# Kernel tuning notes

Measured on AMD Instinct MI355X. Metric: run time of the kernel, lower is better.

Reference implementation:

```python
import jax, jax.numpy as jnp
import numpy as np

HEADS = 16
LN_EPS = 1e-6

def _layernorm(x, scale, bias):
    mu = jnp.mean(x, axis=-1, keepdims=True)
    var = jnp.mean(jnp.square(x - mu), axis=-1, keepdims=True)
    return (x - mu) * jax.lax.rsqrt(var + LN_EPS) * scale + bias

def setup_inputs() -> dict:
    key = jax.random.key(0)
    ks = jax.random.split(key, 5)
    B, L, D, F = 2, 2048, 1024, 4096
    s = lambda fan_in: 1.0 / np.sqrt(fan_in)
    return {
        'x': jax.random.normal(ks[0], (B, L, D), jnp.float32),
        'ln1_scale': jnp.ones((D,), jnp.float32),
        'ln1_bias': jnp.zeros((D,), jnp.float32),
        'w_qkv': jax.random.normal(ks[1], (D, 3 * D), jnp.float32) * s(D),
        'w_proj': jax.random.normal(ks[2], (D, D), jnp.float32) * s(D),
        'b_proj': jnp.zeros((D,), jnp.float32),
        'ln2_scale': jnp.ones((D,), jnp.float32),
        'ln2_bias': jnp.zeros((D,), jnp.float32),
        'w_mlp1': jax.random.normal(ks[3], (D, F), jnp.float32) * s(D),
        'b_mlp1': jnp.zeros((F,), jnp.float32),
        'w_mlp2': jax.random.normal(ks[4], (F, D), jnp.float32) * s(F),
        'b_mlp2': jnp.zeros((D,), jnp.float32),
    }

def reference(x, ln1_scale, ln1_bias, w_qkv, w_proj, b_proj,
              ln2_scale, ln2_bias, w_mlp1, b_mlp1, w_mlp2, b_mlp2):
    B, L, D = x.shape
    H = HEADS
    hd = D // H
    # pre-norm attention
    h = _layernorm(x, ln1_scale, ln1_bias)
    qkv = h @ w_qkv  # [B,L,3D]
    q, k, v = jnp.split(qkv, 3, axis=-1)
    q = q.reshape(B, L, H, hd).transpose(0, 2, 1, 3)  # [B,H,L,hd]
    k = k.reshape(B, L, H, hd).transpose(0, 2, 1, 3)
    v = v.reshape(B, L, H, hd).transpose(0, 2, 1, 3)
    scale = jnp.sqrt(jnp.float32(hd))
    scores = jnp.einsum('bhqd,bhkd->bhqk', q, k) / scale  # [B,H,L,L]
    attn = jax.nn.softmax(scores, axis=-1)
    out = jnp.einsum('bhqk,bhkd->bhqd', attn, v)  # [B,H,L,hd]
    out = out.transpose(0, 2, 1, 3).reshape(B, L, D)
    x = x + out @ w_proj + b_proj
    # pre-norm MLP
    h = _layernorm(x, ln2_scale, ln2_bias)
    m = jax.nn.gelu(h @ w_mlp1 + b_mlp1, approximate=True)
    return x + m @ w_mlp2 + b_mlp2
```

## Files before the change

kernel.cpp:

```cpp
#include <hip/hip_runtime.h>
#include <hip/hip_bf16.h>
#include <cstdint>
#include <cstddef>

typedef __bf16 bf16;
typedef __bf16 bf16x8 __attribute__((ext_vector_type(8)));
typedef float f32x4 __attribute__((ext_vector_type(4)));
typedef short short4v __attribute__((ext_vector_type(4)));
typedef unsigned uint2v __attribute__((ext_vector_type(2)));

#define GLB_AS(p) ((const __attribute__((address_space(1))) unsigned*)(unsigned long long)(p))
#define LDS_AS(p) ((__attribute__((address_space(3))) unsigned*)(unsigned)(unsigned long long)(p))

__device__ __forceinline__ void g2l16(const void* g, void* l) {
  __builtin_amdgcn_global_load_lds(GLB_AS(g), LDS_AS(l), 16, 0, 0);
}

__device__ __forceinline__ short f2bf(float x) {
  bf16 h = (bf16)x;
  return __builtin_bit_cast(short, h);
}

__device__ __forceinline__ unsigned pk_bf16(float a, float b) {
  __hip_bfloat162 h = __float22bfloat162_rn(float2{a, b});
  unsigned u;
  __builtin_memcpy(&u, &h, 4);
  return u;
}

extern "C" __device__ __attribute__((const)) float __ocml_native_exp2_f32(float);
extern "C" __device__ __attribute__((const)) float __ocml_native_recip_f32(float);
__device__ __forceinline__ float fast_exp2(float x) {
  return __ocml_native_exp2_f32(x);
}
__device__ __forceinline__ float fast_tanh(float a) {
  float e = __ocml_native_exp2_f32(a * 2.8853900817779268f);
  return 1.f - 2.f * __ocml_native_recip_f32(e + 1.f);
}

constexpr int MROWS = 4096;
constexpr size_t ATILE = (size_t)MROWS * 32;

#define QSCALE 0.18033688011112042f

__device__ __forceinline__ void transpose_body(
    const float* __restrict__ in, bf16* __restrict__ out, int K, int N,
    int bx, int by, float (*tile)[33], int tid)
{
  int tx = tid & 31, ty = tid >> 5;
  int n0 = bx * 32, k0 = by * 32;
  for (int i = ty; i < 32; i += 8)
    tile[i][tx] = in[(size_t)(k0 + i) * N + n0 + tx];
  __syncthreads();
  bf16* obase = out + (size_t)(k0 >> 5) * N * 32;
  for (int i = ty; i < 32; i += 8)
    obase[(size_t)(n0 + i) * 32 + tx] = (bf16)tile[tx][i];
}

__device__ __forceinline__ void ln_body(
    const float* __restrict__ x, const float* __restrict__ sc,
    const float* __restrict__ bi, bf16* __restrict__ out,
    int row, float* wsum, float* wsq, int tid)
{
  const float* xr = x + (size_t)row * 1024;
  int c = tid * 4;
  float4 xv = *(const float4*)(xr + c);
  float s = xv.x + xv.y + xv.z + xv.w;
  float q = xv.x * xv.x + xv.y * xv.y + xv.z * xv.z + xv.w * xv.w;
#pragma unroll
  for (int off = 1; off < 64; off <<= 1) {
    s += __shfl_xor(s, off);
    q += __shfl_xor(q, off);
  }
  int wv = tid >> 6;
  if ((tid & 63) == 0) { wsum[wv] = s; wsq[wv] = q; }
  __syncthreads();
  s = wsum[0] + wsum[1] + wsum[2] + wsum[3];
  q = wsq[0] + wsq[1] + wsq[2] + wsq[3];
  float mean = s * (1.f / 1024.f);
  float var = q * (1.f / 1024.f) - mean * mean;
  float rstd = rsqrtf(var + 1e-6f);
  float4 scv = *(const float4*)(sc + c);
  float4 biv = *(const float4*)(bi + c);
  bf16* o = out + (size_t)(c >> 5) * ATILE + (size_t)row * 32 + (c & 31);
  o[0] = (bf16)((xv.x - mean) * rstd * scv.x + biv.x);
  o[1] = (bf16)((xv.y - mean) * rstd * scv.y + biv.y);
  o[2] = (bf16)((xv.z - mean) * rstd * scv.z + biv.z);
  o[3] = (bf16)((xv.w - mean) * rstd * scv.w + biv.w);
}

__global__ __launch_bounds__(256) void prep_kernel(
    const float* __restrict__ wqkv, const float* __restrict__ wproj,
    const float* __restrict__ wmlp1, const float* __restrict__ wmlp2,
    bf16* __restrict__ wqkv_t, bf16* __restrict__ wproj_t,
    bf16* __restrict__ wmlp1_t, bf16* __restrict__ wmlp2_t,
    const float* __restrict__ x, const float* __restrict__ ln1s,
    const float* __restrict__ ln1b, bf16* __restrict__ hbuf)
{
  __shared__ float tile[32][33];
  __shared__ float wsum[4], wsq[4];
  int bid = blockIdx.x, tid = threadIdx.x;
  if (bid < 3072)
    transpose_body(wqkv, wqkv_t, 1024, 3072, bid % 96, bid / 96, tile, tid);
  else if (bid < 4096) {
    int i = bid - 3072;
    transpose_body(wproj, wproj_t, 1024, 1024, i % 32, i / 32, tile, tid);
  } else if (bid < 8192) {
    int i = bid - 4096;
    transpose_body(wmlp1, wmlp1_t, 1024, 4096, i % 128, i / 128, tile, tid);
  } else if (bid < 12288) {
    int i = bid - 8192;
    transpose_body(wmlp2, wmlp2_t, 4096, 1024, i % 32, i / 32, tile, tid);
  } else {
    ln_body(x, ln1s, ln1b, hbuf, bid - 12288, wsum, wsq, tid);
  }
}

__global__ __launch_bounds__(256) void ln_kernel(
    const float* __restrict__ x, const float* __restrict__ sc,
    const float* __restrict__ bi, bf16* __restrict__ out)
{
  __shared__ float wsum[4], wsq[4];
  ln_body(x, sc, bi, out, blockIdx.x, wsum, wsq, threadIdx.x);
}

template <int MT, int NT, int KS, int EPI>
__global__ __launch_bounds__(256) void gemm_tt(
    const bf16* __restrict__ A, const bf16* __restrict__ Bt,
    int N, int K,
    const float* __restrict__ bias, const float* __restrict__ resid,
    float* __restrict__ outf, bf16* __restrict__ ob0,
    bf16* __restrict__ ob1, bf16* __restrict__ ob2)
{
  constexpr int TM = MT * 32, TN = NT * 32;
  __shared__ __align__(16) bf16 As[2][TM * 32 * KS];
  __shared__ __align__(16) bf16 Bs[2][TN * 32 * KS];
  const int tid = threadIdx.x, lane = tid & 63, wave = tid >> 6;
  const int wm = wave >> 1, wn = wave & 1;
  const int quad = lane >> 4, l16 = lane & 15;

  int flat = blockIdx.x + gridDim.x * blockIdx.y;
  int xcd = flat & 7, rr = flat >> 3;
  int npx = gridDim.x >> 3;
  int bn = xcd * npx + (rr % npx);
  int bm = rr / npx;

  const size_t astride = ATILE;
  const size_t bstride = (size_t)N * 32;
  const bf16* Abase = A + (size_t)bm * TM * 32 + (size_t)lane * 8;
  const bf16* Bbase = Bt + (size_t)bn * TN * 32 + (size_t)lane * 8;

  f32x4 acc[MT][NT] = {};
  const int KT = K / (32 * KS);

  auto stage = [&](int buf, int kt) {
#pragma unroll
    for (int ks = 0; ks < KS; ks++) {
      const bf16* Ab = Abase + (size_t)(kt * KS + ks) * astride;
      const bf16* Bb = Bbase + (size_t)(kt * KS + ks) * bstride;
#pragma unroll
      for (int i = 0; i < MT / 2; i++)
        g2l16(Ab + (wave + 4 * i) * 512, &As[buf][ks * TM * 32 + (wave + 4 * i) * 512]);
#pragma unroll
      for (int i = 0; i < NT / 2; i++)
        g2l16(Bb + (wave + 4 * i) * 512, &Bs[buf][ks * TN * 32 + (wave + 4 * i) * 512]);
    }
  };

  stage(0, 0);
  int buf = 0;
  for (int kt = 0; kt < KT; kt++) {
    __syncthreads();
    if (kt + 1 < KT) stage(buf ^ 1, kt + 1);
#pragma unroll
    for (int kk = 0; kk < KS; kk++) {
      bf16x8 af[MT], bfr[NT];
#pragma unroll
      for (int mt = 0; mt < MT; mt++)
        af[mt] = *(const bf16x8*)&As[buf][kk * TM * 32 + (wm * MT * 16 + mt * 16 + l16) * 32 + quad * 8];
#pragma unroll
      for (int nt = 0; nt < NT; nt++)
        bfr[nt] = *(const bf16x8*)&Bs[buf][kk * TN * 32 + (wn * NT * 16 + nt * 16 + l16) * 32 + quad * 8];
#pragma unroll
      for (int mt = 0; mt < MT; mt++)
#pragma unroll
        for (int nt = 0; nt < NT; nt++)
          acc[mt][nt] = __builtin_amdgcn_mfma_f32_16x16x32_bf16(af[mt], bfr[nt], acc[mt][nt], 0, 0, 0);
    }
    buf ^= 1;
  }

#pragma unroll
  for (int mt = 0; mt < MT; mt++) {
#pragma unroll
    for (int nt = 0; nt < NT; nt++) {
      int row0 = bm * TM + wm * MT * 16 + mt * 16 + quad * 4;
      int col = bn * TN + wn * NT * 16 + nt * 16 + l16;
      if (EPI == 0) {
        int b = row0 >> 11, l = row0 & 2047;
        int which = col >> 10, d = col & 1023;
        int hh = d >> 6, hdi = d & 63;
        size_t bh = (size_t)(b * 16 + hh);
        if (which == 0) {
#pragma unroll
          for (int r = 0; r < 4; r++)
            ob0[(bh * 2048 + l + r) * 64 + hdi] = (bf16)(acc[mt][nt][r] * QSCALE);
        } else if (which == 1) {
#pragma unroll
          for (int r = 0; r < 4; r++)
            ob1[(bh * 2048 + l + r) * 64 + hdi] = (bf16)acc[mt][nt][r];
        } else {
          short4v v4;
#pragma unroll
          for (int r = 0; r < 4; r++) v4[r] = f2bf(acc[mt][nt][r]);
          *(short4v*)&ob2[(bh * 64 + hdi) * 2048 + l] = v4;
        }
      } else {
#pragma unroll
        for (int r = 0; r < 4; r++) {
          int row = row0 + r;
          float v = acc[mt][nt][r];
          if (EPI == 1) {
            size_t idx = (size_t)row * N + col;
            outf[idx] = v + bias[col] + resid[idx];
          } else {
            float t = v + bias[col];
            float a = 0.7978845608028654f * t * (1.f + 0.044715f * t * t);
            float g = 0.5f * t * (1.f + fast_tanh(a));
            ob0[(size_t)(col >> 5) * ATILE + (size_t)row * 32 + (col & 31)] = (bf16)g;
          }
        }
      }
    }
  }
}

__global__ __launch_bounds__(512, 4) void flash_attn(
    const bf16* __restrict__ Q, const bf16* __restrict__ Kg,
    const bf16* __restrict__ Vg, bf16* __restrict__ O)
{
  __shared__ __align__(16) bf16 Ks[128 * 64];
  __shared__ __align__(16) bf16 Vs[64 * 128];
  const int tid = threadIdx.x, lane = tid & 63, wave = tid >> 6;
  const int quad = lane >> 4, l16 = lane & 15;
  const int qt = blockIdx.x, bh = blockIdx.y;
  const int b = bh >> 4, h = bh & 15;

  const bf16* qg = Q + ((size_t)bh * 2048 + qt * 128) * 64;
  const bf16* kg = Kg + (size_t)bh * 2048 * 64;
  const bf16* vg = Vg + (size_t)bh * 64 * 2048;

  const int kw0 = ((tid >> 3) << 7) + (((tid & 7) << 4) ^ (((tid >> 3) & 7) << 4));
  const int vw0 = ((tid >> 4) << 8) + (((tid & 15) << 4) ^ (((tid >> 4) & 7) << 4));

  bf16x8 qf[2];
#pragma unroll
  for (int kk = 0; kk < 2; kk++)
    qf[kk] = *(const bf16x8*)&qg[(size_t)(wave * 16 + l16) * 64 + kk * 32 + quad * 8];

  f32x4 oacc[4] = {};
  float lrow = 0.f;

  bf16x8 kreg[2], vreg[2];
#pragma unroll
  for (int i = 0; i < 2; i++) {
    int t = tid + i * 512;
    kreg[i] = *(const bf16x8*)&kg[(size_t)(t >> 3) * 64 + (t & 7) * 8];
    vreg[i] = *(const bf16x8*)&vg[(size_t)(t >> 4) * 2048 + (t & 15) * 8];
  }

  for (int kt = 0; kt < 16; kt++) {
    __syncthreads();
#pragma unroll
    for (int i = 0; i < 2; i++) {
      *(bf16x8*)((char*)Ks + kw0 + i * 64 * 128) = kreg[i];
      *(bf16x8*)((char*)Vs + vw0 + i * 32 * 256) = vreg[i];
    }
    __syncthreads();
    if (kt < 15) {
#pragma unroll
      for (int i = 0; i < 2; i++) {
        int t = tid + i * 512;
        kreg[i] = *(const bf16x8*)&kg[((size_t)(kt + 1) * 128 + (t >> 3)) * 64 + (t & 7) * 8];
        vreg[i] = *(const bf16x8*)&vg[(size_t)(t >> 4) * 2048 + (kt + 1) * 128 + (t & 15) * 8];
      }
    }

    f32x4 sacc[8] = {};
    __builtin_amdgcn_s_setprio(1);
#pragma unroll
    for (int kk = 0; kk < 2; kk++) {
#pragma unroll
      for (int ct = 0; ct < 8; ct++) {
        int krow = ct * 16 + l16;
        int kcol = (kk * 64 + quad * 16) ^ ((krow & 7) << 4);
        bf16x8 kf = *(const bf16x8*)((const char*)Ks + krow * 128 + kcol);
        sacc[ct] = __builtin_amdgcn_mfma_f32_16x16x32_bf16(kf, qf[kk], sacc[ct], 0, 0, 0);
      }
    }
    __builtin_amdgcn_s_setprio(0);

    short4v pf[8];
    {
      float sum = 0.f;
#pragma unroll
      for (int ct = 0; ct < 8; ct++) {
        float p0 = fast_exp2(sacc[ct][0]);
        float p1 = fast_exp2(sacc[ct][1]);
        float p2 = fast_exp2(sacc[ct][2]);
        float p3 = fast_exp2(sacc[ct][3]);
        sum += (p0 + p1) + (p2 + p3);
        uint2v u;
        u[0] = pk_bf16(p0, p1);
        u[1] = pk_bf16(p2, p3);
        pf[ct] = __builtin_bit_cast(short4v, u);
      }
      lrow += sum;
    }

    __builtin_amdgcn_s_setprio(1);
#pragma unroll
    for (int ot = 0; ot < 4; ot++) {
#pragma unroll
      for (int ct = 0; ct < 8; ct++) {
        int vrow = ot * 16 + l16;
        int vcol = (ct * 32 + quad * 8) ^ ((vrow & 7) << 4);
        short4v vf = *(const short4v*)((const char*)Vs + vrow * 256 + vcol);
        oacc[ot] = __builtin_amdgcn_mfma_f32_16x16x16bf16_1k(vf, pf[ct], oacc[ot], 0, 0, 0);
      }
    }
    __builtin_amdgcn_s_setprio(0);
  }

  {
    float l = lrow;
    l += __shfl_xor(l, 16);
    l += __shfl_xor(l, 32);
    float inv = 1.f / l;
    int qrow = qt * 128 + wave * 16 + l16;
    size_t grow = (size_t)b * 2048 + qrow;
#pragma unroll
    for (int ot = 0; ot < 4; ot++) {
      int col = h * 64 + ot * 16 + quad * 4;
      short4v o4;
#pragma unroll
      for (int r = 0; r < 4; r++) o4[r] = f2bf(oacc[ot][r] * inv);
      *(short4v*)&O[(size_t)(col >> 5) * ATILE + grow * 32 + (col & 31)] = o4;
    }
  }
}

extern "C" void kernel_launch(void* const* d_in, const int* in_sizes, int n_in,
                              void* d_out, int out_size, void* d_ws, size_t ws_size,
                              hipStream_t stream)
{
  const float* x     = (const float*)d_in[0];
  const float* ln1s  = (const float*)d_in[1];
  const float* ln1b  = (const float*)d_in[2];
  const float* wqkv  = (const float*)d_in[3];
  const float* wproj = (const float*)d_in[4];
  const float* bproj = (const float*)d_in[5];
  const float* ln2s  = (const float*)d_in[6];
  const float* ln2b  = (const float*)d_in[7];
  const float* wmlp1 = (const float*)d_in[8];
  const float* bmlp1 = (const float*)d_in[9];
  const float* wmlp2 = (const float*)d_in[10];
  const float* bmlp2 = (const float*)d_in[11];
  float* out = (float*)d_out;

  char* ws = (char*)d_ws;
  bf16* wqkv_t  = (bf16*)(ws + 0);
  bf16* wproj_t = (bf16*)(ws + 6291456);
  bf16* wmlp1_t = (bf16*)(ws + 8388608);
  bf16* wmlp2_t = (bf16*)(ws + 16777216);
  bf16* hbuf    = (bf16*)(ws + 25165824);
  bf16* qb      = (bf16*)(ws + 33554432);
  bf16* kb      = (bf16*)(ws + 41943040);
  bf16* vb      = (bf16*)(ws + 50331648);
  bf16* aout    = (bf16*)(ws + 58720256);
  bf16* mbuf    = (bf16*)(ws + 33554432);

  prep_kernel<<<16384, 256, 0, stream>>>(wqkv, wproj, wmlp1, wmlp2,
                                         wqkv_t, wproj_t, wmlp1_t, wmlp2_t,
                                         x, ln1s, ln1b, hbuf);
  gemm_tt<4, 4, 1, 0><<<dim3(24, 32), 256, 0, stream>>>(hbuf, wqkv_t, 3072, 1024,
                                                        nullptr, nullptr, nullptr, qb, kb, vb);
  flash_attn<<<dim3(16, 32), 512, 0, stream>>>(qb, kb, vb, aout);
  gemm_tt<2, 4, 2, 1><<<dim3(8, 64), 256, 0, stream>>>(aout, wproj_t, 1024, 1024,
                                                       bproj, x, out, nullptr, nullptr, nullptr);
  ln_kernel<<<4096, 256, 0, stream>>>(out, ln2s, ln2b, hbuf);
  gemm_tt<4, 4, 1, 2><<<dim3(32, 32), 256, 0, stream>>>(hbuf, wmlp1_t, 4096, 1024,
                                                        bmlp1, nullptr, nullptr, mbuf, nullptr, nullptr);
  gemm_tt<2, 4, 2, 1><<<dim3(8, 64), 256, 0, stream>>>(mbuf, wmlp2_t, 1024, 4096,
                                                       bmlp2, out, out, nullptr, nullptr, nullptr);
}
```

Measured before the change: 341.4 us.

## Split attention KV tile across waves with 64-row query blocks and LDS reduction

```diff
diff --git a/kernel.cpp b/kernel.cpp
--- a/kernel.cpp
+++ b/kernel.cpp
@@ -235,14 +235,19 @@
   }
 }
 
-__global__ __launch_bounds__(512, 4) void flash_attn(
+__global__ __launch_bounds__(512, 2) void flash_attn(
     const bf16* __restrict__ Q, const bf16* __restrict__ Kg,
     const bf16* __restrict__ Vg, bf16* __restrict__ O)
 {
-  __shared__ __align__(16) bf16 Ks[128 * 64];
-  __shared__ __align__(16) bf16 Vs[64 * 128];
+  __shared__ __align__(16) char smem[34816];
+  bf16* Ks = (bf16*)smem;
+  bf16* Vs = (bf16*)(smem + 16384);
+  float* obuf = (float*)smem;
+  float* lbuf = (float*)(smem + 32768);
+
   const int tid = threadIdx.x, lane = tid & 63, wave = tid >> 6;
   const int quad = lane >> 4, l16 = lane & 15;
+  const int qi = wave & 1, kp = wave >> 1;
   const int qt = blockIdx.x, bh = blockIdx.y;
   const int b = bh >> 4, h = bh & 15;
 
@@ -253,13 +258,15 @@
   const int kw0 = ((tid >> 3) << 7) + (((tid & 7) << 4) ^ (((tid >> 3) & 7) << 4));
   const int vw0 = ((tid >> 4) << 8) + (((tid & 15) << 4) ^ (((tid >> 4) & 7) << 4));
 
-  bf16x8 qf[2];
-#pragma unroll
-  for (int kk = 0; kk < 2; kk++)
-    qf[kk] = *(const bf16x8*)&qg[(size_t)(wave * 16 + l16) * 64 + kk * 32 + quad * 8];
-
-  f32x4 oacc[4] = {};
-  float lrow = 0.f;
+  bf16x8 qf[4][2];
+#pragma unroll
+  for (int qsub = 0; qsub < 4; qsub++)
+#pragma unroll
+    for (int kk = 0; kk < 2; kk++)
+      qf[qsub][kk] = *(const bf16x8*)&qg[(size_t)(qi * 64 + qsub * 16 + l16) * 64 + kk * 32 + quad * 8];
+
+  f32x4 oacc[4][4] = {};
+  float lrow[4] = {0.f, 0.f, 0.f, 0.f};
 
   bf16x8 kreg[2], vreg[2];
 #pragma unroll
@@ -286,66 +293,122 @@
       }
     }
 
-    f32x4 sacc[8] = {};
+    f32x4 sacc[2][4] = {};
     __builtin_amdgcn_s_setprio(1);
 #pragma unroll
     for (int kk = 0; kk < 2; kk++) {
 #pragma unroll
-      for (int ct = 0; ct < 8; ct++) {
+      for (int ct2 = 0; ct2 < 2; ct2++) {
+        int ct = kp * 2 + ct2;
         int krow = ct * 16 + l16;
         int kcol = (kk * 64 + quad * 16) ^ ((krow & 7) << 4);
         bf16x8 kf = *(const bf16x8*)((const char*)Ks + krow * 128 + kcol);
-        sacc[ct] = __builtin_amdgcn_mfma_f32_16x16x32_bf16(kf, qf[kk], sacc[ct], 0, 0, 0);
+#pragma unroll
+        for (int qsub = 0; qsub < 4; qsub++)
+          sacc[ct2][qsub] = __builtin_amdgcn_mfma_f32_16x16x32_bf16(kf, qf[qsub][kk], sacc[ct2][qsub], 0, 0, 0);
       }
     }
     __builtin_amdgcn_s_setprio(0);
 
-    short4v pf[8];
-    {
-      float sum = 0.f;
-#pragma unroll
-      for (int ct = 0; ct < 8; ct++) {
-        float p0 = fast_exp2(sacc[ct][0]);
-        float p1 = fast_exp2(sacc[ct][1]);
-        float p2 = fast_exp2(sacc[ct][2]);
-        float p3 = fast_exp2(sacc[ct][3]);
-        sum += (p0 + p1) + (p2 + p3);
+    short4v pf[2][4];
+#pragma unroll
+    for (int ct2 = 0; ct2 < 2; ct2++) {
+#pragma unroll
+      for (int qsub = 0; qsub < 4; qsub++) {
+        float p0 = fast_exp2(sacc[ct2][qsub][0]);
+        float p1 = fast_exp2(sacc[ct2][qsub][1]);
+        float p2 = fast_exp2(sacc[ct2][qsub][2]);
+        float p3 = fast_exp2(sacc[ct2][qsub][3]);
+        lrow[qsub] += (p0 + p1) + (p2 + p3);
         uint2v u;
         u[0] = pk_bf16(p0, p1);
         u[1] = pk_bf16(p2, p3);
-        pf[ct] = __builtin_bit_cast(short4v, u);
-      }
-      lrow += sum;
+        pf[ct2][qsub] = __builtin_bit_cast(short4v, u);
+      }
     }
 
     __builtin_amdgcn_s_setprio(1);
 #pragma unroll
     for (int ot = 0; ot < 4; ot++) {
 #pragma unroll
-      for (int ct = 0; ct < 8; ct++) {
+      for (int ct2 = 0; ct2 < 2; ct2++) {
+        int ct = kp * 2 + ct2;
         int vrow = ot * 16 + l16;
         int vcol = (ct * 32 + quad * 8) ^ ((vrow & 7) << 4);
         short4v vf = *(const short4v*)((const char*)Vs + vrow * 256 + vcol);
-        oacc[ot] = __builtin_amdgcn_mfma_f32_16x16x16bf16_1k(vf, pf[ct], oacc[ot], 0, 0, 0);
+#pragma unroll
+        for (int qsub = 0; qsub < 4; qsub++)
+          oacc[ot][qsub] = __builtin_amdgcn_mfma_f32_16x16x16bf16_1k(vf, pf[ct2][qsub], oacc[ot][qsub], 0, 0, 0);
       }
     }
     __builtin_amdgcn_s_setprio(0);
   }
 
+  __syncthreads();
+
   {
-    float l = lrow;
-    l += __shfl_xor(l, 16);
-    l += __shfl_xor(l, 32);
-    float inv = 1.f / l;
-    int qrow = qt * 128 + wave * 16 + l16;
-    size_t grow = (size_t)b * 2048 + qrow;
+    float lr[4];
+#pragma unroll
+    for (int qsub = 0; qsub < 4; qsub++) {
+      float l = lrow[qsub];
+      l += __shfl_xor(l, 16);
+      l += __shfl_xor(l, 32);
+      lr[qsub] = l;
+    }
+    if (quad == 0) {
+#pragma unroll
+      for (int qsub = 0; qsub < 4; qsub++)
+        lbuf[((qi * 4 + kp) * 4 + qsub) * 16 + l16] = lr[qsub];
+    }
+  }
+
+#pragma unroll
+  for (int round = 0; round < 3; round++) {
+    if (kp == round) {
+#pragma unroll
+      for (int ot = 0; ot < 4; ot++) {
+#pragma unroll
+        for (int qsub = 0; qsub < 4; qsub++) {
+          int q = qsub * 16 + l16;
+          int ocol = (ot * 16 + quad * 4) ^ ((q & 7) << 2);
+          f32x4* p = (f32x4*)&obuf[qi * 4096 + q * 64 + ocol];
+          if (round == 0) *p = oacc[ot][qsub];
+          else {
+            f32x4 t = *p;
+            t += oacc[ot][qsub];
+            *p = t;
+          }
+        }
+      }
+    }
+    __syncthreads();
+  }
+
+  if (kp == 3) {
+    float inv[4];
+#pragma unroll
+    for (int qsub = 0; qsub < 4; qsub++) {
+      float s = 0.f;
+#pragma unroll
+      for (int k = 0; k < 4; k++)
+        s += lbuf[((qi * 4 + k) * 4 + qsub) * 16 + l16];
+      inv[qsub] = 1.f / s;
+    }
 #pragma unroll
     for (int ot = 0; ot < 4; ot++) {
       int col = h * 64 + ot * 16 + quad * 4;
-      short4v o4;
-#pragma unroll
-      for (int r = 0; r < 4; r++) o4[r] = f2bf(oacc[ot][r] * inv);
-      *(short4v*)&O[(size_t)(col >> 5) * ATILE + grow * 32 + (col & 31)] = o4;
+#pragma unroll
+      for (int qsub = 0; qsub < 4; qsub++) {
+        int q = qsub * 16 + l16;
+        int ocol = (ot * 16 + quad * 4) ^ ((q & 7) << 2);
+        f32x4 t = *(const f32x4*)&obuf[qi * 4096 + q * 64 + ocol];
+        t += oacc[ot][qsub];
+        short4v o4;
+#pragma unroll
+        for (int r = 0; r < 4; r++) o4[r] = f2bf(t[r] * inv[qsub]);
+        size_t grow = (size_t)b * 2048 + qt * 128 + qi * 64 + q;
+        *(short4v*)&O[(size_t)(col >> 5) * ATILE + grow * 32 + (col & 31)] = o4;
+      }
     }
   }
 }
```

Result: no change. 338.6 us (-0.8%).
